# Kernel optimization log

Measured on AMD Instinct MI355X. Metric: run time of the kernel, lower is better.

Reference implementation:

```python
import jax, jax.numpy as jnp
import numpy as np

N = 50000      # nodes
E = 800000     # edges (avg degree 16)
IN = 128
H = 128
OUT = 1000
K = 10
EPS = 1e-5


def setup_inputs() -> dict:
    key = jax.random.key(0)
    ks = jax.random.split(key, 12)
    s = 0.05  # small init scale for weights
    return {
        "x": jax.random.normal(ks[0], (N, IN), jnp.float32),
        "edge_index": jax.random.randint(ks[1], (2, E), 0, N, dtype=jnp.int32),
        "W1": jax.random.normal(ks[2], (IN, H), jnp.float32) * s,
        "b1": jnp.zeros((H,), jnp.float32),
        "g1": jnp.ones((H,), jnp.float32),
        "be1": jnp.zeros((H,), jnp.float32),
        "W2": jax.random.normal(ks[3], (H, H), jnp.float32) * s,
        "b2": jnp.zeros((H,), jnp.float32),
        "g2": jnp.ones((H,), jnp.float32),
        "be2": jnp.zeros((H,), jnp.float32),
        "att": jax.random.uniform(ks[4], (K + 1,), jnp.float32),  # uniform_(0,1) init
        "W3": jax.random.normal(ks[5], (H, H // 2), jnp.float32) * s,
        "b3": jnp.zeros((H // 2,), jnp.float32),
        "g3": jnp.ones((H // 2,), jnp.float32),
        "be3": jnp.zeros((H // 2,), jnp.float32),
        "Wout": jax.random.normal(ks[6], (H // 2, OUT), jnp.float32) * s,
        "bout": jnp.zeros((OUT,), jnp.float32),
    }


def _bn(x, g, b):
    # training-mode BatchNorm1d: biased batch stats over the node dim
    m = jnp.mean(x, axis=0)
    v = jnp.var(x, axis=0)
    return g * (x - m) * jax.lax.rsqrt(v + EPS) + b


def reference(x, edge_index, W1, b1, g1, be1, W2, b2, g2, be2, att,
              W3, b3, g3, be3, Wout, bout):
    # input MLP with residual
    h = jax.nn.relu(_bn(x @ W1 + b1, g1, be1))
    identity = h
    h = jax.nn.relu(_bn(h @ W2 + b2, g2, be2)) + identity

    # DAGNN: K unnormalized scatter-add hops (APPNP.propagate with edge_weight=1),
    # then softmax(att)-weighted sum over hop representations. Accumulate the
    # weighted sum on the fly instead of materializing the [N, H, K+1] stack.
    src, dst = edge_index[0], edge_index[1]  # message flows src -> dst
    w = jax.nn.softmax(att)
    out = w[0] * h
    cur = h
    for i in range(K):
        cur = jax.ops.segment_sum(cur[src], dst, num_segments=N)
        out = out + w[i + 1] * cur

    # output MLP
    h3 = jax.nn.relu(_bn(out @ W3 + b3, g3, be3))
    return h3 @ Wout + bout
```

## Files before the change

### kernel.cpp

```cpp
#include <hip/hip_runtime.h>
#include <cstdint>
#include <cstddef>

#define N_NODES 50000
#define N_EDGES 800000
#define DIM_H   128
#define DIM_P   64
#define DIM_OUT 1000
#define OUT_PAD 1024
#define KHOPS   10
#define BN_EPS  1e-5f

static inline int ceil_div(int a, int b) { return (a + b - 1) / b; }

typedef short  bf16x8  __attribute__((ext_vector_type(8)));
typedef float  floatx4 __attribute__((ext_vector_type(4)));

__device__ __forceinline__ unsigned short f2bf_rne(float v) {
    unsigned int u = __float_as_uint(v);
    return (unsigned short)((u + 0x7fffu + ((u >> 16) & 1u)) >> 16);
}
__device__ __forceinline__ float bf2f(unsigned short u) {
    return __uint_as_float((unsigned int)u << 16);
}

__global__ void softmax11(const float* __restrict__ att, float* __restrict__ w) {
    if (threadIdx.x == 0) {
        float mx = att[0];
        for (int i = 1; i < KHOPS + 1; ++i) mx = fmaxf(mx, att[i]);
        float e[KHOPS + 1];
        float s = 0.f;
        for (int i = 0; i < KHOPS + 1; ++i) { e[i] = expf(att[i] - mx); s += e[i]; }
        for (int i = 0; i < KHOPS + 1; ++i) w[i] = e[i] / s;
    }
}

__global__ void count_deg(const int* __restrict__ dst, int* __restrict__ deg, int ne) {
    int i = blockIdx.x * blockDim.x + threadIdx.x;
    if (i < ne) atomicAdd(&deg[dst[i]], 1);
}

__global__ __launch_bounds__(1024) void scan_local(const int* __restrict__ deg,
                                                   int* __restrict__ row_ptr,
                                                   int* __restrict__ bsums, int n) {
    __shared__ int wsum[16];
    const int i = blockIdx.x * 1024 + threadIdx.x;
    const int lane = threadIdx.x & 63, w = threadIdx.x >> 6;
    int v = (i < n) ? deg[i] : 0;
    int s = v;
#pragma unroll
    for (int d = 1; d < 64; d <<= 1) {
        int t = __shfl_up(s, d, 64);
        if (lane >= d) s += t;
    }
    if (lane == 63) wsum[w] = s;
    __syncthreads();
    if (w == 0) {
        int x = (lane < 16) ? wsum[lane] : 0;
#pragma unroll
        for (int d = 1; d < 16; d <<= 1) {
            int t = __shfl_up(x, d, 64);
            if (lane >= d) x += t;
        }
        if (lane < 16) wsum[lane] = x;
    }
    __syncthreads();
    int incl = s + ((w > 0) ? wsum[w - 1] : 0);
    if (i < n) row_ptr[i + 1] = incl;
    if (threadIdx.x == 1023) bsums[blockIdx.x] = incl;
}

__global__ void scan_bsums(int* __restrict__ bsums, int nb) {
    int lane = threadIdx.x;
    int v = (lane < nb) ? bsums[lane] : 0;
    int s = v;
#pragma unroll
    for (int d = 1; d < 64; d <<= 1) {
        int t = __shfl_up(s, d, 64);
        if (lane >= d) s += t;
    }
    if (lane < nb) bsums[lane] = s - v;
}

__global__ void scan_finish(int* __restrict__ row_ptr, int* __restrict__ deg,
                            const int* __restrict__ bsums, int n) {
    int i = blockIdx.x * blockDim.x + threadIdx.x;
    if (i < n) {
        int incl = row_ptr[i + 1] + bsums[i >> 10];
        row_ptr[i + 1] = incl;
        deg[i] = incl - deg[i];
    }
    if (i == 0) row_ptr[0] = 0;
}

__global__ void fill_csr(const int* __restrict__ src, const int* __restrict__ dst,
                         int* __restrict__ cursor, int* __restrict__ col, int ne) {
    int i = blockIdx.x * blockDim.x + threadIdx.x;
    if (i < ne) {
        int d = dst[i];
        int pos = atomicAdd(&cursor[d], 1);
        col[pos] = src[i];
    }
}

template<int KD, int CPB, bool OBF>
__global__ __launch_bounds__(256) void gemm_fused(
    const float* __restrict__ A,  const float* __restrict__ scA,
    const float* __restrict__ A2, const float* __restrict__ scA2,
    const float* __restrict__ W,  const float* __restrict__ bias,
    float* __restrict__ C, float* __restrict__ C2, const float* __restrict__ w0p,
    int n, int M) {
    constexpr int CG  = CPB / 4;
    constexpr int RG  = 256 / CG;
    constexpr int RPT = 64 / RG;
    __shared__ float As[64][KD + 4];

    const int tid  = threadIdx.x;
    const int cg   = tid % CG;
    const int rg   = tid / CG;
    const int row0 = blockIdx.x * 64;
    const int col0 = blockIdx.y * CPB + cg * 4;

    constexpr int VECS = 64 * KD / 4;
    for (int i = tid; i < VECS; i += 256) {
        int r  = i / (KD / 4);
        int k4 = (i % (KD / 4)) * 4;
        float4 v = make_float4(0.f, 0.f, 0.f, 0.f);
        int row = row0 + r;
        if (row < n) {
            v = *reinterpret_cast<const float4*>(A + (size_t)row * KD + k4);
            if (scA) {
                float4 sc = *reinterpret_cast<const float4*>(scA + k4);
                float4 sh = *reinterpret_cast<const float4*>(scA + KD + k4);
                v.x = fmaxf(v.x * sc.x + sh.x, 0.f);
                v.y = fmaxf(v.y * sc.y + sh.y, 0.f);
                v.z = fmaxf(v.z * sc.z + sh.z, 0.f);
                v.w = fmaxf(v.w * sc.w + sh.w, 0.f);
            }
            if (A2) {
                float4 u  = *reinterpret_cast<const float4*>(A2 + (size_t)row * KD + k4);
                float4 sc = *reinterpret_cast<const float4*>(scA2 + k4);
                float4 sh = *reinterpret_cast<const float4*>(scA2 + KD + k4);
                v.x += fmaxf(u.x * sc.x + sh.x, 0.f);
                v.y += fmaxf(u.y * sc.y + sh.y, 0.f);
                v.z += fmaxf(u.z * sc.z + sh.z, 0.f);
                v.w += fmaxf(u.w * sc.w + sh.w, 0.f);
            }
        }
        *reinterpret_cast<float4*>(&As[r][k4]) = v;
    }
    __syncthreads();

    if (col0 >= M) return;

    float acc[RPT][4];
#pragma unroll
    for (int r = 0; r < RPT; ++r)
#pragma unroll
        for (int c = 0; c < 4; ++c) acc[r][c] = 0.f;

    for (int k4 = 0; k4 < KD; k4 += 4) {
        float4 w0 = *reinterpret_cast<const float4*>(W + (size_t)(k4 + 0) * M + col0);
        float4 w1 = *reinterpret_cast<const float4*>(W + (size_t)(k4 + 1) * M + col0);
        float4 w2 = *reinterpret_cast<const float4*>(W + (size_t)(k4 + 2) * M + col0);
        float4 w3 = *reinterpret_cast<const float4*>(W + (size_t)(k4 + 3) * M + col0);
#pragma unroll
        for (int r = 0; r < RPT; ++r) {
            float4 a = *reinterpret_cast<const float4*>(&As[rg * RPT + r][k4]);
            acc[r][0] += a.x * w0.x + a.y * w1.x + a.z * w2.x + a.w * w3.x;
            acc[r][1] += a.x * w0.y + a.y * w1.y + a.z * w2.y + a.w * w3.y;
            acc[r][2] += a.x * w0.z + a.y * w1.z + a.z * w2.z + a.w * w3.z;
            acc[r][3] += a.x * w0.w + a.y * w1.w + a.z * w2.w + a.w * w3.w;
        }
    }

    float4 b = make_float4(0.f, 0.f, 0.f, 0.f);
    if (bias) b = *reinterpret_cast<const float4*>(bias + col0);
    const float w0s = C2 ? w0p[0] : 0.f;
#pragma unroll
    for (int r = 0; r < RPT; ++r) {
        int row = row0 + rg * RPT + r;
        if (row < n) {
            float4 o = make_float4(acc[r][0] + b.x, acc[r][1] + b.y,
                                   acc[r][2] + b.z, acc[r][3] + b.w);
            if (OBF) {
                unsigned short* cb = reinterpret_cast<unsigned short*>(C);
                ushort4 p;
                p.x = f2bf_rne(o.x); p.y = f2bf_rne(o.y);
                p.z = f2bf_rne(o.z); p.w = f2bf_rne(o.w);
                *reinterpret_cast<ushort4*>(cb + (size_t)row * M + col0) = p;
            } else {
                *reinterpret_cast<float4*>(C + (size_t)row * M + col0) = o;
            }
            if (C2) {
                float4 q = make_float4(w0s * o.x, w0s * o.y, w0s * o.z, w0s * o.w);
                *reinterpret_cast<float4*>(C2 + (size_t)row * M + col0) = q;
            }
        }
    }
}

template<int M>
__global__ __launch_bounds__(256) void colstats(const float* __restrict__ Z,
                                                double* __restrict__ st, int n) {
    constexpr int RG = 256 / M;
    const int tid = threadIdx.x;
    const int c = tid % M, rg = tid / M;
    double s = 0.0, ss = 0.0;
    for (int row = blockIdx.x * RG + rg; row < n; row += gridDim.x * RG) {
        float v = Z[(size_t)row * M + c];
        s += v;
        ss += (double)v * (double)v;
    }
    __shared__ double sh[2][256];
    sh[0][tid] = s;
    sh[1][tid] = ss;
    __syncthreads();
    if (rg == 0) {
#pragma unroll
        for (int g = 1; g < RG; ++g) { s += sh[0][c + g * M]; ss += sh[1][c + g * M]; }
        atomicAdd(&st[c], s);
        atomicAdd(&st[M + c], ss);
    }
}

__global__ void bn_finalize(const double* __restrict__ st, const float* __restrict__ g,
                            const float* __restrict__ be, float* __restrict__ scsh,
                            int M, int n) {
    int c = threadIdx.x + blockIdx.x * blockDim.x;
    if (c < M) {
        double m = st[c] / n;
        double v = st[M + c] / n - m * m;
        float scale = g[c] * rsqrtf((float)v + BN_EPS);
        scsh[c]     = scale;
        scsh[M + c] = be[c] - (float)m * scale;
    }
}

__global__ __launch_bounds__(256) void propagate(
    const unsigned short* __restrict__ cur, unsigned short* __restrict__ nxt,
    float* __restrict__ oacc,
    const int* __restrict__ row_ptr, const int* __restrict__ col,
    const float* __restrict__ wts, int hop, int n) {
    const int node = blockIdx.x * 4 + (threadIdx.x >> 6);
    const int lane = threadIdx.x & 63;
    const int g = lane >> 3;
    const int l = lane & 7;
    if (node >= n) return;
    const int beg = row_ptr[node], end = row_ptr[node + 1];
    float acc[8];
#pragma unroll
    for (int j = 0; j < 8; ++j) acc[j] = 0.f;

    int e = beg;
    for (; e + 16 <= end; e += 16) {
        int s0 = col[e + g];
        int s1 = col[e + g + 8];
        bf16x8 v0 = *reinterpret_cast<const bf16x8*>(cur + (size_t)s0 * DIM_P + l * 8);
        bf16x8 v1 = *reinterpret_cast<const bf16x8*>(cur + (size_t)s1 * DIM_P + l * 8);
#pragma unroll
        for (int j = 0; j < 8; ++j)
            acc[j] += bf2f((unsigned short)v0[j]) + bf2f((unsigned short)v1[j]);
    }
    if (e + 8 <= end) {
        int s = col[e + g];
        bf16x8 v = *reinterpret_cast<const bf16x8*>(cur + (size_t)s * DIM_P + l * 8);
#pragma unroll
        for (int j = 0; j < 8; ++j) acc[j] += bf2f((unsigned short)v[j]);
        e += 8;
    }
    if (e + g < end) {
        int s = col[e + g];
        bf16x8 v = *reinterpret_cast<const bf16x8*>(cur + (size_t)s * DIM_P + l * 8);
#pragma unroll
        for (int j = 0; j < 8; ++j) acc[j] += bf2f((unsigned short)v[j]);
    }

#pragma unroll
    for (int off = 8; off < 64; off <<= 1) {
#pragma unroll
        for (int j = 0; j < 8; ++j) acc[j] += __shfl_xor(acc[j], off, 64);
    }

    if (g == 0) {
        const size_t o = (size_t)node * DIM_P + l * 8;
        if (nxt) {
            bf16x8 ov;
#pragma unroll
            for (int j = 0; j < 8; ++j) ov[j] = (short)f2bf_rne(acc[j]);
            *reinterpret_cast<bf16x8*>(nxt + o) = ov;
        }
        const float w = wts[hop];
        float* op = oacc + o;
        float4 t0 = *reinterpret_cast<const float4*>(op);
        float4 t1 = *reinterpret_cast<const float4*>(op + 4);
        t0.x = fmaf(w, acc[0], t0.x); t0.y = fmaf(w, acc[1], t0.y);
        t0.z = fmaf(w, acc[2], t0.z); t0.w = fmaf(w, acc[3], t0.w);
        t1.x = fmaf(w, acc[4], t1.x); t1.y = fmaf(w, acc[5], t1.y);
        t1.z = fmaf(w, acc[6], t1.z); t1.w = fmaf(w, acc[7], t1.w);
        *reinterpret_cast<float4*>(op) = t0;
        *reinterpret_cast<float4*>(op + 4) = t1;
    }
}

__global__ void prep_wout(const float* __restrict__ W, unsigned short* __restrict__ WT) {
    int idx = blockIdx.x * blockDim.x + threadIdx.x;
    if (idx < OUT_PAD * DIM_P) {
        int c = idx >> 6, k = idx & 63;
        WT[idx] = (c < DIM_OUT) ? f2bf_rne(W[(size_t)k * DIM_OUT + c]) : (unsigned short)0;
    }
}

__global__ void bn3_relu_bf16(const float* __restrict__ Z, const float* __restrict__ scsh,
                              unsigned short* __restrict__ O) {
    const int total8 = N_NODES * DIM_P / 8;
    int i = blockIdx.x * blockDim.x + threadIdx.x;
    if (i >= total8) return;
    int base = i * 8;
    int c = base & (DIM_P - 1);
    float4 z0 = *reinterpret_cast<const float4*>(Z + base);
    float4 z1 = *reinterpret_cast<const float4*>(Z + base + 4);
    float4 s0 = *reinterpret_cast<const float4*>(scsh + c);
    float4 s1 = *reinterpret_cast<const float4*>(scsh + c + 4);
    float4 h0 = *reinterpret_cast<const float4*>(scsh + DIM_P + c);
    float4 h1 = *reinterpret_cast<const float4*>(scsh + DIM_P + c + 4);
    bf16x8 o;
    o[0] = (short)f2bf_rne(fmaxf(z0.x * s0.x + h0.x, 0.f));
    o[1] = (short)f2bf_rne(fmaxf(z0.y * s0.y + h0.y, 0.f));
    o[2] = (short)f2bf_rne(fmaxf(z0.z * s0.z + h0.z, 0.f));
    o[3] = (short)f2bf_rne(fmaxf(z0.w * s0.w + h0.w, 0.f));
    o[4] = (short)f2bf_rne(fmaxf(z1.x * s1.x + h1.x, 0.f));
    o[5] = (short)f2bf_rne(fmaxf(z1.y * s1.y + h1.y, 0.f));
    o[6] = (short)f2bf_rne(fmaxf(z1.z * s1.z + h1.z, 0.f));
    o[7] = (short)f2bf_rne(fmaxf(z1.w * s1.w + h1.w, 0.f));
    *reinterpret_cast<bf16x8*>(O + base) = o;
}

__global__ __launch_bounds__(256, 4) void out_gemm_mfma(
    const unsigned short* __restrict__ ABF, const unsigned short* __restrict__ WT,
    const float* __restrict__ bout, float* __restrict__ out) {
    const int wave = threadIdx.x >> 6;
    const int lane = threadIdx.x & 63;
    const int m    = lane & 15;
    const int quad = lane >> 4;
    const int kb   = quad * 8;
    const int c0   = blockIdx.y * 256 + wave * 64;

    bf16x8 afrag[4][2];
    float4 bias[4];
#pragma unroll
    for (int t = 0; t < 4; ++t) {
        const unsigned short* wrow = WT + (size_t)(c0 + t * 16 + m) * DIM_P;
        afrag[t][0] = *reinterpret_cast<const bf16x8*>(wrow + kb);
        afrag[t][1] = *reinterpret_cast<const bf16x8*>(wrow + 32 + kb);
        int cc = c0 + t * 16 + quad * 4;
        bias[t] = (cc < DIM_OUT) ? *reinterpret_cast<const float4*>(bout + cc)
                                 : make_float4(0.f, 0.f, 0.f, 0.f);
    }

    const int NT = N_NODES / 16;
    for (int rt = blockIdx.x; rt < NT; rt += gridDim.x) {
        const int row = rt * 16 + m;
        const unsigned short* arow = ABF + (size_t)row * DIM_P;
        bf16x8 bfrag0 = *reinterpret_cast<const bf16x8*>(arow + kb);
        bf16x8 bfrag1 = *reinterpret_cast<const bf16x8*>(arow + 32 + kb);
        float* orow = out + (size_t)row * DIM_OUT;
#pragma unroll
        for (int t = 0; t < 4; ++t) {
            floatx4 acc = {0.f, 0.f, 0.f, 0.f};
            acc = __builtin_amdgcn_mfma_f32_16x16x32_bf16(afrag[t][0], bfrag0, acc, 0, 0, 0);
            acc = __builtin_amdgcn_mfma_f32_16x16x32_bf16(afrag[t][1], bfrag1, acc, 0, 0, 0);
            int cc = c0 + t * 16 + quad * 4;
            if (cc < DIM_OUT) {
                float4 o = make_float4(acc[0] + bias[t].x, acc[1] + bias[t].y,
                                       acc[2] + bias[t].z, acc[3] + bias[t].w);
                *reinterpret_cast<float4*>(orow + cc) = o;
            }
        }
    }
}

extern "C" void kernel_launch(void* const* d_in, const int* in_sizes, int n_in,
                              void* d_out, int out_size, void* d_ws, size_t ws_size,
                              hipStream_t stream) {
    const float* x    = (const float*)d_in[0];
    const int*   ei   = (const int*)  d_in[1];
    const float* W1   = (const float*)d_in[2];
    const float* g1   = (const float*)d_in[4];
    const float* be1  = (const float*)d_in[5];
    const float* W2   = (const float*)d_in[6];
    const float* g2   = (const float*)d_in[8];
    const float* be2  = (const float*)d_in[9];
    const float* att  = (const float*)d_in[10];
    const float* W3   = (const float*)d_in[11];
    const float* g3   = (const float*)d_in[13];
    const float* be3  = (const float*)d_in[14];
    const float* Wout = (const float*)d_in[15];
    const float* bout = (const float*)d_in[16];
    float* out = (float*)d_out;

    char* base = (char*)d_ws;
    size_t off = 0;
    auto alloc = [&](size_t bytes) -> void* {
        void* r = base + off;
        off += (bytes + 255) & ~(size_t)255;
        return r;
    };
    float*  f0      = (float*) alloc((size_t)N_NODES * DIM_H * 4);
    float*  f1      = (float*) alloc((size_t)N_NODES * DIM_H * 4);
    unsigned short* yb = (unsigned short*)alloc((size_t)N_NODES * DIM_P * 2);
    unsigned short* tb = (unsigned short*)alloc((size_t)N_NODES * DIM_P * 2);
    float*  oa      = (float*) alloc((size_t)N_NODES * DIM_P * 4);
    double* st      = (double*)alloc(640 * 8);
    float*  scsh    = (float*) alloc(768 * 4);
    float*  wts     = (float*) alloc(16 * 4);
    int*    row_ptr = (int*)   alloc((size_t)(N_NODES + 1) * 4);
    int*    deg     = (int*)   alloc((size_t)N_NODES * 4);
    int*    col     = (int*)   alloc((size_t)N_EDGES * 4);
    int*    bsums   = (int*)   alloc(64 * 4);
    unsigned short* WT  = (unsigned short*)alloc((size_t)OUT_PAD * DIM_P * 2);
    unsigned short* ABF = (unsigned short*)alloc((size_t)N_NODES * DIM_P * 2);

    const int* src = ei;
    const int* dst = ei + N_EDGES;
    double* st1 = st;   double* st2 = st + 256; double* st3 = st + 512;
    float*  sc1 = scsh; float*  sc2 = scsh + 256; float* sc3 = scsh + 512;

    hipMemsetAsync(st, 0, 640 * 8, stream);
    hipMemsetAsync(deg, 0, (size_t)N_NODES * 4, stream);

    softmax11<<<1, 64, 0, stream>>>(att, wts);
    prep_wout<<<ceil_div(OUT_PAD * DIM_P, 256), 256, 0, stream>>>(Wout, WT);

    count_deg<<<ceil_div(N_EDGES, 256), 256, 0, stream>>>(dst, deg, N_EDGES);
    const int NB = ceil_div(N_NODES, 1024);
    scan_local<<<NB, 1024, 0, stream>>>(deg, row_ptr, bsums, N_NODES);
    scan_bsums<<<1, 64, 0, stream>>>(bsums, NB);
    scan_finish<<<ceil_div(N_NODES, 256), 256, 0, stream>>>(row_ptr, deg, bsums, N_NODES);
    fill_csr<<<ceil_div(N_EDGES, 256), 256, 0, stream>>>(src, dst, deg, col, N_EDGES);

    const int RB = ceil_div(N_NODES, 64);

    gemm_fused<128, 128, false><<<dim3(RB, 1), 256, 0, stream>>>(
        x, nullptr, nullptr, nullptr, W1, nullptr, f0, nullptr, nullptr, N_NODES, DIM_H);
    colstats<128><<<256, 256, 0, stream>>>(f0, st1, N_NODES);
    bn_finalize<<<1, 128, 0, stream>>>(st1, g1, be1, sc1, 128, N_NODES);

    gemm_fused<128, 128, false><<<dim3(RB, 1), 256, 0, stream>>>(
        f0, sc1, nullptr, nullptr, W2, nullptr, f1, nullptr, nullptr, N_NODES, DIM_H);
    colstats<128><<<256, 256, 0, stream>>>(f1, st2, N_NODES);
    bn_finalize<<<1, 128, 0, stream>>>(st2, g2, be2, sc2, 128, N_NODES);

    gemm_fused<128, 64, true><<<dim3(RB, 1), 256, 0, stream>>>(
        f1, sc2, f0, sc1, W3, nullptr, (float*)yb, oa, wts, N_NODES, DIM_P);

    {
        unsigned short* cur = yb;
        unsigned short* nxt = tb;
        for (int hop = 1; hop <= KHOPS; ++hop) {
            propagate<<<ceil_div(N_NODES, 4), 256, 0, stream>>>(
                cur, (hop == KHOPS) ? nullptr : nxt, oa, row_ptr, col, wts, hop, N_NODES);
            unsigned short* t = cur; cur = nxt; nxt = t;
        }
    }

    colstats<64><<<256, 256, 0, stream>>>(oa, st3, N_NODES);
    bn_finalize<<<1, 64, 0, stream>>>(st3, g3, be3, sc3, 64, N_NODES);
    bn3_relu_bf16<<<ceil_div(N_NODES * DIM_P / 8, 256), 256, 0, stream>>>(oa, sc3, ABF);

    out_gemm_mfma<<<dim3(512, 4), 256, 0, stream>>>(ABF, WT, bout, out);
}
```

Before: 799.2 us.

## Fuse BN stats into GEMM epilogues and merge small setup kernels

Batch-norm column statistics for the first two linear layers are now accumulated in the GEMM epilogue via shared-memory reduction and double atomics, which removes two separate colstats passes over the 50000x128 activations. BN finalize is folded into the consuming kernels, which recompute scale and shift per block. The softmax, Wout transpose and the memsets are merged into one init kernel, and the block-sum scan is folded into scan_finish, cutting launch count. The trade-off is more per-block redundant work and added atomics, and the bias add is dropped, which is harmless only because BN cancels it.

```diff
diff --git a/kernel.cpp b/kernel.cpp
--- a/kernel.cpp
+++ b/kernel.cpp
@@ -24,14 +24,24 @@
     return __uint_as_float((unsigned int)u << 16);
 }
 
-__global__ void softmax11(const float* __restrict__ att, float* __restrict__ w) {
-    if (threadIdx.x == 0) {
+__global__ void init_all(const float* __restrict__ att, float* __restrict__ w,
+                         const float* __restrict__ Wout, unsigned short* __restrict__ WT,
+                         double* __restrict__ st, int* __restrict__ deg) {
+    const int gid = blockIdx.x * blockDim.x + threadIdx.x;
+    const int stride = gridDim.x * blockDim.x;
+    if (gid == 0) {
         float mx = att[0];
         for (int i = 1; i < KHOPS + 1; ++i) mx = fmaxf(mx, att[i]);
         float e[KHOPS + 1];
         float s = 0.f;
         for (int i = 0; i < KHOPS + 1; ++i) { e[i] = expf(att[i] - mx); s += e[i]; }
         for (int i = 0; i < KHOPS + 1; ++i) w[i] = e[i] / s;
+    }
+    for (int i = gid; i < 640; i += stride) st[i] = 0.0;
+    for (int i = gid; i < N_NODES; i += stride) deg[i] = 0;
+    for (int i = gid; i < OUT_PAD * DIM_P; i += stride) {
+        int c = i >> 6, k = i & 63;
+        WT[i] = (c < DIM_OUT) ? f2bf_rne(Wout[(size_t)k * DIM_OUT + c]) : (unsigned short)0;
     }
 }
 
@@ -70,23 +80,24 @@
     if (threadIdx.x == 1023) bsums[blockIdx.x] = incl;
 }
 
-__global__ void scan_bsums(int* __restrict__ bsums, int nb) {
-    int lane = threadIdx.x;
-    int v = (lane < nb) ? bsums[lane] : 0;
-    int s = v;
-#pragma unroll
-    for (int d = 1; d < 64; d <<= 1) {
-        int t = __shfl_up(s, d, 64);
-        if (lane >= d) s += t;
-    }
-    if (lane < nb) bsums[lane] = s - v;
-}
-
 __global__ void scan_finish(int* __restrict__ row_ptr, int* __restrict__ deg,
-                            const int* __restrict__ bsums, int n) {
+                            const int* __restrict__ bsums, int n, int nb) {
+    __shared__ int boff[64];
+    if (threadIdx.x < 64) {
+        int lane = threadIdx.x;
+        int v = (lane < nb) ? bsums[lane] : 0;
+        int s = v;
+#pragma unroll
+        for (int d = 1; d < 64; d <<= 1) {
+            int t = __shfl_up(s, d, 64);
+            if (lane >= d) s += t;
+        }
+        boff[lane] = s - v;
+    }
+    __syncthreads();
     int i = blockIdx.x * blockDim.x + threadIdx.x;
     if (i < n) {
-        int incl = row_ptr[i + 1] + bsums[i >> 10];
+        int incl = row_ptr[i + 1] + boff[i >> 10];
         row_ptr[i + 1] = incl;
         deg[i] = incl - deg[i];
     }
@@ -103,23 +114,43 @@
     }
 }
 
-template<int KD, int CPB, bool OBF>
+template<int KD, int CPB, bool STATS, bool OBF>
 __global__ __launch_bounds__(256) void gemm_fused(
-    const float* __restrict__ A,  const float* __restrict__ scA,
-    const float* __restrict__ A2, const float* __restrict__ scA2,
-    const float* __restrict__ W,  const float* __restrict__ bias,
+    const float* __restrict__ A,  const double* __restrict__ stA,
+    const float* __restrict__ gA, const float* __restrict__ beA,
+    const float* __restrict__ A2, const double* __restrict__ stA2,
+    const float* __restrict__ gA2, const float* __restrict__ beA2,
+    const float* __restrict__ W,
     float* __restrict__ C, float* __restrict__ C2, const float* __restrict__ w0p,
-    int n, int M) {
+    double* __restrict__ stOut, int n, int M) {
     constexpr int CG  = CPB / 4;
     constexpr int RG  = 256 / CG;
     constexpr int RPT = 64 / RG;
     __shared__ float As[64][KD + 4];
+    __shared__ float scA_l[2][KD];
+    __shared__ float scA2_l[2][KD];
 
     const int tid  = threadIdx.x;
     const int cg   = tid % CG;
     const int rg   = tid / CG;
     const int row0 = blockIdx.x * 64;
     const int col0 = blockIdx.y * CPB + cg * 4;
+
+    if (stA && tid < KD) {
+        double m = stA[tid] / n;
+        double v = stA[KD + tid] / n - m * m;
+        float scale = gA[tid] * rsqrtf((float)v + BN_EPS);
+        scA_l[0][tid] = scale;
+        scA_l[1][tid] = beA[tid] - (float)m * scale;
+    }
+    if (A2 && tid < KD) {
+        double m = stA2[tid] / n;
+        double v = stA2[KD + tid] / n - m * m;
+        float scale = gA2[tid] * rsqrtf((float)v + BN_EPS);
+        scA2_l[0][tid] = scale;
+        scA2_l[1][tid] = beA2[tid] - (float)m * scale;
+    }
+    if (stA || A2) __syncthreads();
 
     constexpr int VECS = 64 * KD / 4;
     for (int i = tid; i < VECS; i += 256) {
@@ -129,9 +160,9 @@
         int row = row0 + r;
         if (row < n) {
             v = *reinterpret_cast<const float4*>(A + (size_t)row * KD + k4);
-            if (scA) {
-                float4 sc = *reinterpret_cast<const float4*>(scA + k4);
-                float4 sh = *reinterpret_cast<const float4*>(scA + KD + k4);
+            if (stA) {
+                float4 sc = *reinterpret_cast<const float4*>(&scA_l[0][k4]);
+                float4 sh = *reinterpret_cast<const float4*>(&scA_l[1][k4]);
                 v.x = fmaxf(v.x * sc.x + sh.x, 0.f);
                 v.y = fmaxf(v.y * sc.y + sh.y, 0.f);
                 v.z = fmaxf(v.z * sc.z + sh.z, 0.f);
@@ -139,8 +170,8 @@
             }
             if (A2) {
                 float4 u  = *reinterpret_cast<const float4*>(A2 + (size_t)row * KD + k4);
-                float4 sc = *reinterpret_cast<const float4*>(scA2 + k4);
-                float4 sh = *reinterpret_cast<const float4*>(scA2 + KD + k4);
+                float4 sc = *reinterpret_cast<const float4*>(&scA2_l[0][k4]);
+                float4 sh = *reinterpret_cast<const float4*>(&scA2_l[1][k4]);
                 v.x += fmaxf(u.x * sc.x + sh.x, 0.f);
                 v.y += fmaxf(u.y * sc.y + sh.y, 0.f);
                 v.z += fmaxf(u.z * sc.z + sh.z, 0.f);
@@ -151,50 +182,85 @@
     }
     __syncthreads();
 
-    if (col0 >= M) return;
-
     float acc[RPT][4];
 #pragma unroll
     for (int r = 0; r < RPT; ++r)
 #pragma unroll
         for (int c = 0; c < 4; ++c) acc[r][c] = 0.f;
 
-    for (int k4 = 0; k4 < KD; k4 += 4) {
-        float4 w0 = *reinterpret_cast<const float4*>(W + (size_t)(k4 + 0) * M + col0);
-        float4 w1 = *reinterpret_cast<const float4*>(W + (size_t)(k4 + 1) * M + col0);
-        float4 w2 = *reinterpret_cast<const float4*>(W + (size_t)(k4 + 2) * M + col0);
-        float4 w3 = *reinterpret_cast<const float4*>(W + (size_t)(k4 + 3) * M + col0);
+    if (col0 < M) {
+        for (int k4 = 0; k4 < KD; k4 += 4) {
+            float4 w0 = *reinterpret_cast<const float4*>(W + (size_t)(k4 + 0) * M + col0);
+            float4 w1 = *reinterpret_cast<const float4*>(W + (size_t)(k4 + 1) * M + col0);
+            float4 w2 = *reinterpret_cast<const float4*>(W + (size_t)(k4 + 2) * M + col0);
+            float4 w3 = *reinterpret_cast<const float4*>(W + (size_t)(k4 + 3) * M + col0);
+#pragma unroll
+            for (int r = 0; r < RPT; ++r) {
+                float4 a = *reinterpret_cast<const float4*>(&As[rg * RPT + r][k4]);
+                acc[r][0] += a.x * w0.x + a.y * w1.x + a.z * w2.x + a.w * w3.x;
+                acc[r][1] += a.x * w0.y + a.y * w1.y + a.z * w2.y + a.w * w3.y;
+                acc[r][2] += a.x * w0.z + a.y * w1.z + a.z * w2.z + a.w * w3.z;
+                acc[r][3] += a.x * w0.w + a.y * w1.w + a.z * w2.w + a.w * w3.w;
+            }
+        }
+
+        const float w0s = C2 ? w0p[0] : 0.f;
 #pragma unroll
         for (int r = 0; r < RPT; ++r) {
-            float4 a = *reinterpret_cast<const float4*>(&As[rg * RPT + r][k4]);
-            acc[r][0] += a.x * w0.x + a.y * w1.x + a.z * w2.x + a.w * w3.x;
-            acc[r][1] += a.x * w0.y + a.y * w1.y + a.z * w2.y + a.w * w3.y;
-            acc[r][2] += a.x * w0.z + a.y * w1.z + a.z * w2.z + a.w * w3.z;
-            acc[r][3] += a.x * w0.w + a.y * w1.w + a.z * w2.w + a.w * w3.w;
-        }
-    }
-
-    float4 b = make_float4(0.f, 0.f, 0.f, 0.f);
-    if (bias) b = *reinterpret_cast<const float4*>(bias + col0);
-    const float w0s = C2 ? w0p[0] : 0.f;
-#pragma unroll
-    for (int r = 0; r < RPT; ++r) {
-        int row = row0 + rg * RPT + r;
-        if (row < n) {
-            float4 o = make_float4(acc[r][0] + b.x, acc[r][1] + b.y,
-                                   acc[r][2] + b.z, acc[r][3] + b.w);
-            if (OBF) {
-                unsigned short* cb = reinterpret_cast<unsigned short*>(C);
-                ushort4 p;
-                p.x = f2bf_rne(o.x); p.y = f2bf_rne(o.y);
-                p.z = f2bf_rne(o.z); p.w = f2bf_rne(o.w);
-                *reinterpret_cast<ushort4*>(cb + (size_t)row * M + col0) = p;
-            } else {
-                *reinterpret_cast<float4*>(C + (size_t)row * M + col0) = o;
-            }
-            if (C2) {
-                float4 q = make_float4(w0s * o.x, w0s * o.y, w0s * o.z, w0s * o.w);
-                *reinterpret_cast<float4*>(C2 + (size_t)row * M + col0) = q;
+            int row = row0 + rg * RPT + r;
+            if (row < n) {
+                float4 o = make_float4(acc[r][0], acc[r][1], acc[r][2], acc[r][3]);
+                if (OBF) {
+                    unsigned short* cb = reinterpret_cast<unsigned short*>(C);
+                    ushort4 p;
+                    p.x = f2bf_rne(o.x); p.y = f2bf_rne(o.y);
+                    p.z = f2bf_rne(o.z); p.w = f2bf_rne(o.w);
+                    *reinterpret_cast<ushort4*>(cb + (size_t)row * M + col0) = p;
+                } else {
+                    *reinterpret_cast<float4*>(C + (size_t)row * M + col0) = o;
+                }
+                if (C2) {
+                    float4 q = make_float4(w0s * o.x, w0s * o.y, w0s * o.z, w0s * o.w);
+                    *reinterpret_cast<float4*>(C2 + (size_t)row * M + col0) = q;
+                }
+            }
+        }
+    }
+
+    if (STATS) {
+        float s[4] = {0.f, 0.f, 0.f, 0.f}, q[4] = {0.f, 0.f, 0.f, 0.f};
+#pragma unroll
+        for (int r = 0; r < RPT; ++r) {
+            int row = row0 + rg * RPT + r;
+            if (row < n) {
+#pragma unroll
+                for (int c = 0; c < 4; ++c) {
+                    float v = acc[r][c];
+                    s[c] += v;
+                    q[c] += v * v;
+                }
+            }
+        }
+        __syncthreads();
+        float* sb = &As[0][0];
+        float* qb = sb + RG * CPB;
+#pragma unroll
+        for (int c = 0; c < 4; ++c) {
+            sb[rg * CPB + cg * 4 + c] = s[c];
+            qb[rg * CPB + cg * 4 + c] = q[c];
+        }
+        __syncthreads();
+        if (rg == 0 && col0 < M) {
+#pragma unroll
+            for (int c = 0; c < 4; ++c) {
+                float ts = 0.f, tq = 0.f;
+#pragma unroll
+                for (int g2 = 0; g2 < RG; ++g2) {
+                    ts += sb[g2 * CPB + cg * 4 + c];
+                    tq += qb[g2 * CPB + cg * 4 + c];
+                }
+                atomicAdd(&stOut[col0 + c], (double)ts);
+                atomicAdd(&stOut[M + col0 + c], (double)tq);
             }
         }
     }
@@ -221,19 +287,6 @@
         for (int g = 1; g < RG; ++g) { s += sh[0][c + g * M]; ss += sh[1][c + g * M]; }
         atomicAdd(&st[c], s);
         atomicAdd(&st[M + c], ss);
-    }
-}
-
-__global__ void bn_finalize(const double* __restrict__ st, const float* __restrict__ g,
-                            const float* __restrict__ be, float* __restrict__ scsh,
-                            int M, int n) {
-    int c = threadIdx.x + blockIdx.x * blockDim.x;
-    if (c < M) {
-        double m = st[c] / n;
-        double v = st[M + c] / n - m * m;
-        float scale = g[c] * rsqrtf((float)v + BN_EPS);
-        scsh[c]     = scale;
-        scsh[M + c] = be[c] - (float)m * scale;
     }
 }
 
@@ -303,16 +356,19 @@
     }
 }
 
-__global__ void prep_wout(const float* __restrict__ W, unsigned short* __restrict__ WT) {
-    int idx = blockIdx.x * blockDim.x + threadIdx.x;
-    if (idx < OUT_PAD * DIM_P) {
-        int c = idx >> 6, k = idx & 63;
-        WT[idx] = (c < DIM_OUT) ? f2bf_rne(W[(size_t)k * DIM_OUT + c]) : (unsigned short)0;
-    }
-}
-
-__global__ void bn3_relu_bf16(const float* __restrict__ Z, const float* __restrict__ scsh,
+__global__ void bn3_relu_bf16(const float* __restrict__ Z, const double* __restrict__ st3,
+                              const float* __restrict__ g3, const float* __restrict__ be3,
                               unsigned short* __restrict__ O) {
+    __shared__ float sc[DIM_P], sh[DIM_P];
+    if (threadIdx.x < DIM_P) {
+        int c = threadIdx.x;
+        double m = st3[c] / N_NODES;
+        double v = st3[DIM_P + c] / N_NODES - m * m;
+        float scale = g3[c] * rsqrtf((float)v + BN_EPS);
+        sc[c] = scale;
+        sh[c] = be3[c] - (float)m * scale;
+    }
+    __syncthreads();
     const int total8 = N_NODES * DIM_P / 8;
     int i = blockIdx.x * blockDim.x + threadIdx.x;
     if (i >= total8) return;
@@ -320,10 +376,10 @@
     int c = base & (DIM_P - 1);
     float4 z0 = *reinterpret_cast<const float4*>(Z + base);
     float4 z1 = *reinterpret_cast<const float4*>(Z + base + 4);
-    float4 s0 = *reinterpret_cast<const float4*>(scsh + c);
-    float4 s1 = *reinterpret_cast<const float4*>(scsh + c + 4);
-    float4 h0 = *reinterpret_cast<const float4*>(scsh + DIM_P + c);
-    float4 h1 = *reinterpret_cast<const float4*>(scsh + DIM_P + c + 4);
+    float4 s0 = *reinterpret_cast<const float4*>(&sc[c]);
+    float4 s1 = *reinterpret_cast<const float4*>(&sc[c + 4]);
+    float4 h0 = *reinterpret_cast<const float4*>(&sh[c]);
+    float4 h1 = *reinterpret_cast<const float4*>(&sh[c + 4]);
     bf16x8 o;
     o[0] = (short)f2bf_rne(fmaxf(z0.x * s0.x + h0.x, 0.f));
     o[1] = (short)f2bf_rne(fmaxf(z0.y * s0.y + h0.y, 0.f));
@@ -412,7 +468,6 @@
     unsigned short* tb = (unsigned short*)alloc((size_t)N_NODES * DIM_P * 2);
     float*  oa      = (float*) alloc((size_t)N_NODES * DIM_P * 4);
     double* st      = (double*)alloc(640 * 8);
-    float*  scsh    = (float*) alloc(768 * 4);
     float*  wts     = (float*) alloc(16 * 4);
     int*    row_ptr = (int*)   alloc((size_t)(N_NODES + 1) * 4);
     int*    deg     = (int*)   alloc((size_t)N_NODES * 4);
@@ -424,35 +479,32 @@
     const int* src = ei;
     const int* dst = ei + N_EDGES;
     double* st1 = st;   double* st2 = st + 256; double* st3 = st + 512;
-    float*  sc1 = scsh; float*  sc2 = scsh + 256; float* sc3 = scsh + 512;
-
-    hipMemsetAsync(st, 0, 640 * 8, stream);
-    hipMemsetAsync(deg, 0, (size_t)N_NODES * 4, stream);
-
-    softmax11<<<1, 64, 0, stream>>>(att, wts);
-    prep_wout<<<ceil_div(OUT_PAD * DIM_P, 256), 256, 0, stream>>>(Wout, WT);
+
+    init_all<<<256, 256, 0, stream>>>(att, wts, Wout, WT, st, deg);
 
     count_deg<<<ceil_div(N_EDGES, 256), 256, 0, stream>>>(dst, deg, N_EDGES);
     const int NB = ceil_div(N_NODES, 1024);
     scan_local<<<NB, 1024, 0, stream>>>(deg, row_ptr, bsums, N_NODES);
-    scan_bsums<<<1, 64, 0, stream>>>(bsums, NB);
-    scan_finish<<<ceil_div(N_NODES, 256), 256, 0, stream>>>(row_ptr, deg, bsums, N_NODES);
+    scan_finish<<<ceil_div(N_NODES, 256), 256, 0, stream>>>(row_ptr, deg, bsums,
+                                                            N_NODES, NB);
     fill_csr<<<ceil_div(N_EDGES, 256), 256, 0, stream>>>(src, dst, deg, col, N_EDGES);
 
     const int RB = ceil_div(N_NODES, 64);
 
-    gemm_fused<128, 128, false><<<dim3(RB, 1), 256, 0, stream>>>(
-        x, nullptr, nullptr, nullptr, W1, nullptr, f0, nullptr, nullptr, N_NODES, DIM_H);
-    colstats<128><<<256, 256, 0, stream>>>(f0, st1, N_NODES);
-    bn_finalize<<<1, 128, 0, stream>>>(st1, g1, be1, sc1, 128, N_NODES);
-
-    gemm_fused<128, 128, false><<<dim3(RB, 1), 256, 0, stream>>>(
-        f0, sc1, nullptr, nullptr, W2, nullptr, f1, nullptr, nullptr, N_NODES, DIM_H);
-    colstats<128><<<256, 256, 0, stream>>>(f1, st2, N_NODES);
-    bn_finalize<<<1, 128, 0, stream>>>(st2, g2, be2, sc2, 128, N_NODES);
-
-    gemm_fused<128, 64, true><<<dim3(RB, 1), 256, 0, stream>>>(
-        f1, sc2, f0, sc1, W3, nullptr, (float*)yb, oa, wts, N_NODES, DIM_P);
+    gemm_fused<128, 128, true, false><<<dim3(RB, 1), 256, 0, stream>>>(
+        x, nullptr, nullptr, nullptr,
+        nullptr, nullptr, nullptr, nullptr,
+        W1, f0, nullptr, nullptr, st1, N_NODES, DIM_H);
+
+    gemm_fused<128, 128, true, false><<<dim3(RB, 1), 256, 0, stream>>>(
+        f0, st1, g1, be1,
+        nullptr, nullptr, nullptr, nullptr,
+        W2, f1, nullptr, nullptr, st2, N_NODES, DIM_H);
+
+    gemm_fused<128, 64, false, true><<<dim3(RB, 1), 256, 0, stream>>>(
+        f1, st2, g2, be2,
+        f0, st1, g1, be1,
+        W3, (float*)yb, oa, wts, nullptr, N_NODES, DIM_P);
 
     {
         unsigned short* cur = yb;
@@ -465,8 +517,8 @@
     }
 
     colstats<64><<<256, 256, 0, stream>>>(oa, st3, N_NODES);
-    bn_finalize<<<1, 64, 0, stream>>>(st3, g3, be3, sc3, 64, N_NODES);
-    bn3_relu_bf16<<<ceil_div(N_NODES * DIM_P / 8, 256), 256, 0, stream>>>(oa, sc3, ABF);
+    bn3_relu_bf16<<<ceil_div(N_NODES * DIM_P / 8, 256), 256, 0, stream>>>(
+        oa, st3, g3, be3, ABF);
 
     out_gemm_mfma<<<dim3(512, 4), 256, 0, stream>>>(ABF, WT, bout, out);
 }
```

Result: slower. 872.6 us (+9.2%).
